# Kernel optimization log

Hardware: AMD Instinct MI355X
Metric: run time of the kernel (lower is better)

Reference implementation:

```python
import jax, jax.numpy as jnp
from jax import lax
import numpy as np

FEAT_STRIDE = 16
PRE_NMS_TOP_N = 2000
POST_NMS_TOP_N = 300
NMS_THRESH = 0.7


def _whctrs(a):
    w = a[2] - a[0] + 1.0
    h = a[3] - a[1] + 1.0
    return w, h, a[0] + 0.5 * (w - 1.0), a[1] + 0.5 * (h - 1.0)


def _mkanchors(ws, hs, x_ctr, y_ctr):
    ws = np.asarray(ws, dtype=np.float64)
    hs = np.asarray(hs, dtype=np.float64)
    return np.stack([x_ctr - 0.5 * (ws - 1.0), y_ctr - 0.5 * (hs - 1.0),
                     x_ctr + 0.5 * (ws - 1.0), y_ctr + 0.5 * (hs - 1.0)], axis=1)


def generate_anchors(base_size=16, ratios=np.array([0.5, 1.0, 2.0]), scales=np.array([8.0, 16.0, 32.0])):
    base = np.array([1.0, 1.0, float(base_size), float(base_size)]) - 1.0
    w, h, xc, yc = _whctrs(base)
    size = w * h
    ws = np.round(np.sqrt(size / ratios))
    hs = np.round(ws * ratios)
    ratio_anchors = _mkanchors(ws, hs, xc, yc)
    out = []
    for i in range(ratio_anchors.shape[0]):
        w_i, h_i, xc_i, yc_i = _whctrs(ratio_anchors[i])
        out.append(_mkanchors(w_i * scales, h_i * scales, xc_i, yc_i))
    return np.vstack(out).astype(np.float32)


ANCHORS = generate_anchors()  # [A=9, 4]
NUM_ANCHORS = ANCHORS.shape[0]


def _nms_keep(boxes, thresh):
    # boxes [N,4], already sorted by descending score; torchvision IoU convention.
    x1, y1, x2, y2 = boxes[:, 0], boxes[:, 1], boxes[:, 2], boxes[:, 3]
    areas = (x2 - x1) * (y2 - y1)
    xx1 = jnp.maximum(x1[:, None], x1[None, :])
    yy1 = jnp.maximum(y1[:, None], y1[None, :])
    xx2 = jnp.minimum(x2[:, None], x2[None, :])
    yy2 = jnp.minimum(y2[:, None], y2[None, :])
    inter = jnp.clip(xx2 - xx1, 0.0) * jnp.clip(yy2 - yy1, 0.0)
    iou = inter / (areas[:, None] + areas[None, :] - inter + 1e-9)
    n = boxes.shape[0]
    # sup[i, j] True => box i (higher score) suppresses later box j
    sup = (iou > thresh) & jnp.triu(jnp.ones((n, n), bool), 1)

    def body(i, keep):
        return keep & ~(keep[i] & sup[i])

    return lax.fori_loop(0, n, body, jnp.ones((n,), bool))


def setup_inputs() -> dict:
    key = jax.random.key(0)
    k1, k2 = jax.random.split(key)
    B, A, H, W = 8, NUM_ANCHORS, 128, 128
    scores = jax.random.normal(k1, (B, 2 * A, H, W), jnp.float32)
    bbox_deltas = jax.random.normal(k2, (B, 4 * A, H, W), jnp.float32) * 0.2
    im_h = float(H * FEAT_STRIDE)
    im_w = float(W * FEAT_STRIDE)
    im_info = jnp.tile(jnp.array([[im_h, im_w, 1.0]], jnp.float32), (B, 1))
    return {"scores": scores, "bbox_deltas": bbox_deltas, "im_info": im_info}


def reference(scores, bbox_deltas, im_info):
    B, _, H, W = scores.shape
    A = NUM_ANCHORS
    # --- anchor generation over the feature grid ---
    sx = jnp.arange(W, dtype=jnp.float32) * FEAT_STRIDE
    sy = jnp.arange(H, dtype=jnp.float32) * FEAT_STRIDE
    gx, gy = jnp.meshgrid(sx, sy)  # 'xy' indexing matches np.meshgrid default
    shifts = jnp.stack([gx.ravel(), gy.ravel(), gx.ravel(), gy.ravel()], axis=1)  # [K,4]
    anchors = (jnp.asarray(ANCHORS)[None, :, :] + shifts[:, None, :]).reshape(-1, 4)  # [K*A,4]

    obj_scores = scores[:, A:].transpose(0, 2, 3, 1).reshape(B, -1)   # [B, K*A]
    deltas = bbox_deltas.transpose(0, 2, 3, 1).reshape(B, -1, 4)      # [B, K*A, 4]

    # --- bbox_transform_inv ---
    widths = anchors[:, 2] - anchors[:, 0] + 1.0
    heights = anchors[:, 3] - anchors[:, 1] + 1.0
    ctr_x = anchors[:, 0] + 0.5 * widths
    ctr_y = anchors[:, 1] + 0.5 * heights
    dx, dy, dw, dh = deltas[..., 0], deltas[..., 1], deltas[..., 2], deltas[..., 3]
    pred_ctr_x = dx * widths + ctr_x
    pred_ctr_y = dy * heights + ctr_y
    pred_w = jnp.exp(dw) * widths
    pred_h = jnp.exp(dh) * heights
    proposals = jnp.stack([pred_ctr_x - 0.5 * pred_w, pred_ctr_y - 0.5 * pred_h,
                           pred_ctr_x + 0.5 * pred_w, pred_ctr_y + 0.5 * pred_h], axis=-1)

    # --- clip_boxes: im_info[b] = (h, w, scale) ---
    max_x = (im_info[:, 1] - 1.0)[:, None]
    max_y = (im_info[:, 0] - 1.0)[:, None]
    proposals = jnp.stack([
        jnp.clip(proposals[..., 0], 0.0, max_x),
        jnp.clip(proposals[..., 1], 0.0, max_y),
        jnp.clip(proposals[..., 2], 0.0, max_x),
        jnp.clip(proposals[..., 3], 0.0, max_y)], axis=-1)

    # --- pre-NMS top-k by score ---
    _, order = lax.top_k(obj_scores, PRE_NMS_TOP_N)                  # [B, pre]
    top_props = jnp.take_along_axis(proposals, order[..., None], axis=1)  # [B, pre, 4]

    # --- per-image greedy NMS (fixed-size, jit-compatible) ---
    keep = jax.vmap(lambda b: _nms_keep(b, NMS_THRESH))(top_props)   # [B, pre] bool
    sel = jnp.argsort(jnp.where(keep, 0, 1), axis=1, stable=True)[:, :POST_NMS_TOP_N]
    valid = jnp.take_along_axis(keep, sel, axis=1)                   # [B, post]
    out_boxes = jnp.take_along_axis(top_props, sel[..., None], axis=1) * valid[..., None].astype(top_props.dtype)

    batch_idx = jnp.broadcast_to(
        jnp.arange(B, dtype=out_boxes.dtype)[:, None, None], (B, POST_NMS_TOP_N, 1))
    return jnp.concatenate([batch_idx, out_boxes], axis=-1)  # [B, post_nms_topN, 5]
```

## Files before the change

### kernel.cpp

```cpp
#include <hip/hip_runtime.h>

#define NB 8
#define NA 9
#define HH 128
#define WW 128
#define NCELL (HH * WW)
#define NTOT (NCELL * NA)
#define PRE_K 2000
#define POST_K 300
#define CAP 4096
#define HBLK 9
#define NMS_TH 0.7f

__constant__ float c_aw[NA] = {184.f, 368.f, 736.f, 128.f, 256.f, 512.f, 88.f, 176.f, 352.f};
__constant__ float c_ah[NA] = {96.f, 192.f, 384.f, 128.f, 256.f, 512.f, 176.f, 352.f, 704.f};

__device__ __forceinline__ unsigned int sortable(float s) {
    unsigned int u = __float_as_uint(s);
    return (u & 0x80000000u) ? ~u : (u | 0x80000000u);
}

__device__ __forceinline__ unsigned long long shflx64(unsigned long long v, int m) {
    return __shfl_xor(v, m, 64);
}

__global__ __launch_bounds__(1024) void hist0_kernel(const float* __restrict__ scores,
                                                     unsigned int* __restrict__ h0out) {
    __shared__ unsigned int h[2048];
    int b = blockIdx.y, tid = threadIdx.x;
    h[tid] = 0; h[tid + 1024] = 0;
    __syncthreads();
    const float4* sp4 = (const float4*)(scores + (size_t)b * 18 * NCELL + (size_t)NA * NCELL);
    int base4 = blockIdx.x * 4096;
#pragma unroll
    for (int e = 0; e < 4; ++e) {
        float4 v = sp4[base4 + e * 1024 + tid];
        atomicAdd(&h[sortable(v.x) >> 21], 1u);
        atomicAdd(&h[sortable(v.y) >> 21], 1u);
        atomicAdd(&h[sortable(v.z) >> 21], 1u);
        atomicAdd(&h[sortable(v.w) >> 21], 1u);
    }
    __syncthreads();
    unsigned int* o = h0out + ((size_t)(b * HBLK + blockIdx.x)) * 2048;
    o[tid] = h[tid];
    o[tid + 1024] = h[tid + 1024];
}

__global__ __launch_bounds__(1024) void select0_kernel(const unsigned int* __restrict__ h0out,
                                                       uint2* __restrict__ state0,
                                                       unsigned int* __restrict__ gh1,
                                                       int* __restrict__ cnt) {
    __shared__ unsigned int thr[1024];
    int b = blockIdx.x, tid = threadIdx.x;
    if (tid < 128) gh1[b * 128 + tid] = 0;
    if (tid == 0) cnt[b] = 0;
    unsigned int c0 = 0, c1 = 0;
    for (int p = 0; p < HBLK; ++p) {
        const unsigned int* hp = h0out + ((size_t)(b * HBLK + p)) * 2048;
        uint2 v = *(const uint2*)&hp[2 * tid];
        c0 += v.x; c1 += v.y;
    }
    thr[tid] = c0 + c1;
    __syncthreads();
    for (int off = 1; off < 1024; off <<= 1) {
        unsigned int v = (tid + off < 1024) ? thr[tid + off] : 0u;
        __syncthreads();
        thr[tid] += v;
        __syncthreads();
    }
    unsigned int above = (tid < 1023) ? thr[tid + 1] : 0u;
    if (thr[tid] >= (unsigned)PRE_K && above < (unsigned)PRE_K) {
        if (above + c1 >= (unsigned)PRE_K)
            state0[b] = make_uint2((unsigned)(2 * tid + 1), (unsigned)(PRE_K)-above);
        else
            state0[b] = make_uint2((unsigned)(2 * tid), (unsigned)(PRE_K)-above - c1);
    }
}

__global__ __launch_bounds__(1024) void hist1_kernel(const float* __restrict__ scores,
                                                     const uint2* __restrict__ state0,
                                                     unsigned int* __restrict__ gh1) {
    __shared__ unsigned int h[128];
    int b = blockIdx.y, tid = threadIdx.x;
    if (tid < 128) h[tid] = 0;
    __syncthreads();
    unsigned int piv = state0[b].x;
    const float4* sp4 = (const float4*)(scores + (size_t)b * 18 * NCELL + (size_t)NA * NCELL);
    int base4 = blockIdx.x * 4096;
#pragma unroll
    for (int e = 0; e < 4; ++e) {
        float4 v = sp4[base4 + e * 1024 + tid];
        unsigned int u;
        u = sortable(v.x); if ((u >> 21) == piv) atomicAdd(&h[(u >> 14) & 127u], 1u);
        u = sortable(v.y); if ((u >> 21) == piv) atomicAdd(&h[(u >> 14) & 127u], 1u);
        u = sortable(v.z); if ((u >> 21) == piv) atomicAdd(&h[(u >> 14) & 127u], 1u);
        u = sortable(v.w); if ((u >> 21) == piv) atomicAdd(&h[(u >> 14) & 127u], 1u);
    }
    __syncthreads();
    if (tid < 128 && h[tid]) atomicAdd(&gh1[b * 128 + tid], h[tid]);
}

__global__ void select1_kernel(const unsigned int* __restrict__ gh1,
                               const uint2* __restrict__ state0,
                               unsigned int* __restrict__ state1) {
    int b = blockIdx.x, lane = threadIdx.x;
    unsigned int c0 = 0, c1 = 0;
    if (lane < 64) {
        c0 = gh1[b * 128 + 2 * lane];
        c1 = gh1[b * 128 + 2 * lane + 1];
    }
    unsigned int sum = c0 + c1;
#pragma unroll
    for (int off = 1; off < 64; off <<= 1) {
        unsigned int v = __shfl_down(sum, off, 64);
        if (lane + off < 64) sum += v;
    }
    unsigned int above = __shfl_down(sum, 1, 64);
    if (lane == 63) above = 0;
    unsigned int need0 = state0[b].y;
    if (sum >= need0 && above < need0) {
        unsigned int d = (above + c1 >= need0) ? (unsigned)(2 * lane + 1) : (unsigned)(2 * lane);
        unsigned int prefix = (state0[b].x << 7) | d;
        state1[b] = prefix << 14;
    }
}

__global__ void gather_kernel(const float* __restrict__ scores,
                              const unsigned int* __restrict__ state1,
                              int* __restrict__ cnt,
                              unsigned long long* __restrict__ buf) {
    __shared__ unsigned long long lbuf[2048];
    __shared__ int lcnt;
    __shared__ int gbase;
    int b = blockIdx.y;
    int tid = threadIdx.x;
    if (tid == 0) lcnt = 0;
    __syncthreads();
    unsigned int P = state1[b];
    const float4* sp4 = (const float4*)(scores + (size_t)b * 18 * NCELL + (size_t)NA * NCELL);
    int base4 = blockIdx.x * 512;
#pragma unroll
    for (int e = 0; e < 2; ++e) {
        int t4 = base4 + e * 256 + tid;
        float4 v = sp4[t4];
        float el[4] = {v.x, v.y, v.z, v.w};
#pragma unroll
        for (int j = 0; j < 4; ++j) {
            unsigned int u = sortable(el[j]);
            if (u >= P) {
                int idx4 = t4 * 4 + j;
                int a = idx4 >> 14;
                int cell = idx4 & 16383;
                unsigned int i = (unsigned int)cell * 9u + (unsigned int)a;
                int pos = atomicAdd(&lcnt, 1);
                lbuf[pos] = ((unsigned long long)u << 32) |
                            (unsigned long long)(0xFFFFFFFFu - i);
            }
        }
    }
    __syncthreads();
    if (tid == 0) gbase = atomicAdd(&cnt[b], lcnt);
    __syncthreads();
    int m = lcnt, gb = gbase;
    for (int t = tid; t < m; t += 256) {
        int g = gb + t;
        if (g < CAP) buf[(size_t)b * CAP + g] = lbuf[t];
    }
}

#define SHFL_STEP(J)                                                          \
    {                                                                         \
        int d_ = (J) >> 1;                                                    \
        bool keepMax = (((tid & d_) == 0) == (((2u * (unsigned)tid) & k) == 0)); \
        unsigned long long pa = shflx64(va, d_);                              \
        unsigned long long pb = shflx64(vb, d_);                              \
        va = keepMax ? (va > pa ? va : pa) : (va < pa ? va : pa);             \
        vb = keepMax ? (vb > pb ? vb : pb) : (vb < pb ? vb : pb);             \
    }
#define LOCAL_STEP()                                                          \
    {                                                                         \
        bool desc = (((2u * (unsigned)tid) & k) == 0);                        \
        unsigned long long lo = va < vb ? va : vb;                            \
        unsigned long long hi = va < vb ? vb : va;                            \
        va = desc ? hi : lo; vb = desc ? lo : hi;                             \
    }

__global__ __launch_bounds__(1024) void sort_kernel(const unsigned long long* __restrict__ buf,
                                                    const int* __restrict__ cnt,
                                                    unsigned int* __restrict__ topidx) {
    __shared__ unsigned long long s[CAP];
    int b = blockIdx.x;
    int tid = threadIdx.x;
    int n = min(cnt[b], CAP);
    const unsigned long long* src = buf + (size_t)b * CAP;
    if (n <= 2048) {
        unsigned long long va = (2 * tid < n) ? src[2 * tid] : 0ULL;
        unsigned long long vb = (2 * tid + 1 < n) ? src[2 * tid + 1] : 0ULL;
#pragma unroll
        for (unsigned k = 2; k <= 128; k <<= 1) {
#pragma unroll
            for (unsigned j = k >> 1; j >= 2; j >>= 1) SHFL_STEP(j)
            LOCAL_STEP()
        }
        for (unsigned k = 256; k <= 2048; k <<= 1) {
            s[2 * tid] = va; s[2 * tid + 1] = vb;
            __syncthreads();
            for (unsigned j = k >> 1; j >= 128; j >>= 1) {
                for (int t = tid; t < 2048; t += 1024) {
                    int ixj = t ^ (int)j;
                    if (ixj > t) {
                        unsigned long long x = s[t], y = s[ixj];
                        if ((((unsigned)t & k) == 0) ? (x < y) : (x > y)) { s[t] = y; s[ixj] = x; }
                    }
                }
                __syncthreads();
            }
            va = s[2 * tid]; vb = s[2 * tid + 1];
#pragma unroll
            for (unsigned j = 64; j >= 2; j >>= 1) SHFL_STEP(j)
            LOCAL_STEP()
        }
        s[2 * tid] = va; s[2 * tid + 1] = vb;
        __syncthreads();
    } else {
        for (int t = tid; t < CAP; t += 1024)
            s[t] = (t < n) ? src[t] : 0ULL;
        __syncthreads();
        for (int k = 2; k <= CAP; k <<= 1) {
            for (int j = k >> 1; j > 0; j >>= 1) {
                for (int t = tid; t < CAP; t += 1024) {
                    int ixj = t ^ j;
                    if (ixj > t) {
                        unsigned long long x = s[t], y = s[ixj];
                        if (((t & k) == 0) ? (x < y) : (x > y)) { s[t] = y; s[ixj] = x; }
                    }
                }
                __syncthreads();
            }
        }
    }
    for (int r = tid; r < PRE_K; r += 1024)
        topidx[(size_t)b * PRE_K + r] = 0xFFFFFFFFu - (unsigned int)(s[r] & 0xFFFFFFFFu);
}

__global__ void decode_kernel(const unsigned int* __restrict__ topidx,
                              const float* __restrict__ deltas,
                              const float* __restrict__ im_info,
                              float4* __restrict__ props) {
    int gid = blockIdx.x * 256 + threadIdx.x;
    if (gid >= NB * PRE_K) return;
    int b = gid / PRE_K;
    unsigned int i = topidx[gid];
    unsigned int cell = i / 9u;
    unsigned int a = i - cell * 9u;
    int wx = (int)(cell & 127u), hy = (int)(cell >> 7);
    const float* dp = deltas + (size_t)b * 36 * NCELL + (size_t)(4u * a) * NCELL +
                      (size_t)hy * WW + wx;
    float dx = dp[0];
    float dy = dp[NCELL];
    float dw = dp[2 * NCELL];
    float dh = dp[3 * NCELL];
    float W_ = c_aw[a], H_ = c_ah[a];
    float cx = (float)(16 * wx + 8), cy = (float)(16 * hy + 8);
    float px = __fadd_rn(__fmul_rn(dx, W_), cx);
    float py = __fadd_rn(__fmul_rn(dy, H_), cy);
    float pw = __fmul_rn((float)exp((double)dw), W_);
    float ph = __fmul_rn((float)exp((double)dh), H_);
    float hw = __fmul_rn(0.5f, pw), hh = __fmul_rn(0.5f, ph);
    float x1 = __fsub_rn(px, hw), y1 = __fsub_rn(py, hh);
    float x2 = __fadd_rn(px, hw), y2 = __fadd_rn(py, hh);
    float maxx = __fsub_rn(im_info[b * 3 + 1], 1.0f);
    float maxy = __fsub_rn(im_info[b * 3 + 0], 1.0f);
    x1 = fminf(fmaxf(x1, 0.0f), maxx);
    y1 = fminf(fmaxf(y1, 0.0f), maxy);
    x2 = fminf(fmaxf(x2, 0.0f), maxx);
    y2 = fminf(fmaxf(y2, 0.0f), maxy);
    props[gid] = make_float4(x1, y1, x2, y2);
}

__global__ void mask_kernel(const float4* __restrict__ boxes,
                            unsigned long long* __restrict__ colm) {
    int iT = blockIdx.x, jT = blockIdx.y, b = blockIdx.z;
    if (iT > jT) return;
    __shared__ float4 ib[64];
    int t = threadIdx.x;
    int i0 = iT * 64;
    ib[t] = (i0 + t < PRE_K) ? boxes[(size_t)b * PRE_K + i0 + t] : make_float4(0.f, 0.f, -1.f, -1.f);
    __syncthreads();
    int j = jT * 64 + t;
    if (j >= PRE_K) return;
    float4 jb = boxes[(size_t)b * PRE_K + j];
    float barea = __fmul_rn(__fsub_rn(jb.z, jb.x), __fsub_rn(jb.w, jb.y));
    unsigned long long m = 0ULL;
    for (int ii = 0; ii < 64; ++ii) {
        int i = i0 + ii;
        if (i < j) {
            float4 c = ib[ii];
            float aarea = __fmul_rn(__fsub_rn(c.z, c.x), __fsub_rn(c.w, c.y));
            float xx1 = fmaxf(c.x, jb.x), yy1 = fmaxf(c.y, jb.y);
            float xx2 = fminf(c.z, jb.z), yy2 = fminf(c.w, jb.w);
            float iw = fmaxf(__fsub_rn(xx2, xx1), 0.0f);
            float ih = fmaxf(__fsub_rn(yy2, yy1), 0.0f);
            float inter = __fmul_rn(iw, ih);
            float denom = __fadd_rn(__fsub_rn(__fadd_rn(aarea, barea), inter), 1e-9f);
            float iou = __fdiv_rn(inter, denom);
            if (iou > NMS_TH) m |= (1ULL << ii);
        }
    }
    colm[((size_t)b * 32 + iT) * 2048 + j] = m;
}

__global__ void scan_kernel(const unsigned long long* __restrict__ colm,
                            const float4* __restrict__ boxes,
                            float* __restrict__ out) {
    int b = blockIdx.x;
    int lane = threadIdx.x;
    __shared__ unsigned long long kw[32];
    __shared__ int keeplist[POST_K];
    const unsigned long long* cb = colm + (size_t)b * 32 * 2048;
    int total = 0;
    bool done = false;
    for (int k = 0; k < 32 && !done; ++k) {
        int j = k * 64 + lane;
        unsigned long long d = 0;
        int w = 0;
        for (; w + 4 <= k; w += 4) {
            unsigned long long a0 = cb[(size_t)(w + 0) * 2048 + j] & kw[w + 0];
            unsigned long long a1 = cb[(size_t)(w + 1) * 2048 + j] & kw[w + 1];
            unsigned long long a2 = cb[(size_t)(w + 2) * 2048 + j] & kw[w + 2];
            unsigned long long a3 = cb[(size_t)(w + 3) * 2048 + j] & kw[w + 3];
            d |= (a0 | a1) | (a2 | a3);
        }
        for (; w < k; ++w) d |= cb[(size_t)w * 2048 + j] & kw[w];
        unsigned long long diag = cb[(size_t)k * 2048 + j];
        bool alive_me = (d == 0ULL) && (j < PRE_K);
        unsigned long long alive = __ballot(alive_me);
        unsigned long long keptw = 0ULL;
        while (alive) {
            int i = __builtin_ctzll(alive);
            keptw |= (1ULL << i);
            if (lane == 0) keeplist[total] = k * 64 + i;
            total++;
            if (total >= POST_K) { done = true; break; }
            unsigned long long sup = __ballot(((diag >> i) & 1ULL) != 0ULL);
            alive &= ~sup;
            alive &= ~keptw;
        }
        if (lane == 0) kw[k] = keptw;
        __syncthreads();
    }
    __syncthreads();
    int K = min(total, POST_K);
    const float4* bb = boxes + (size_t)b * PRE_K;
    for (int r = lane; r < POST_K; r += 64) {
        float4 v = make_float4(0.f, 0.f, 0.f, 0.f);
        if (r < K) v = bb[keeplist[r]];
        float* o = out + ((size_t)b * POST_K + r) * 5;
        o[0] = (float)b;
        o[1] = v.x;
        o[2] = v.y;
        o[3] = v.z;
        o[4] = v.w;
    }
}

extern "C" void kernel_launch(void* const* d_in, const int* in_sizes, int n_in,
                              void* d_out, int out_size, void* d_ws, size_t ws_size,
                              hipStream_t stream) {
    const float* scores = (const float*)d_in[0];
    const float* deltas = (const float*)d_in[1];
    const float* im_info = (const float*)d_in[2];
    float* out = (float*)d_out;
    char* ws = (char*)d_ws;

    unsigned int* h0out = (unsigned int*)(ws + 0);
    unsigned int* gh1 = (unsigned int*)(ws + 589824);
    uint2* state0 = (uint2*)(ws + 593920);
    unsigned int* state1 = (unsigned int*)(ws + 593984);
    int* cnt = (int*)(ws + 594048);
    unsigned long long* buf = (unsigned long long*)(ws + 594112);
    unsigned int* topidx = (unsigned int*)(ws + 856256);
    float4* props = (float4*)(ws + 920256);
    unsigned long long* colm = (unsigned long long*)(ws + 1176320);

    hipLaunchKernelGGL(hist0_kernel, dim3(HBLK, NB), dim3(1024), 0, stream, scores, h0out);
    hipLaunchKernelGGL(select0_kernel, dim3(NB), dim3(1024), 0, stream, h0out, state0, gh1, cnt);
    hipLaunchKernelGGL(hist1_kernel, dim3(HBLK, NB), dim3(1024), 0, stream, scores, state0, gh1);
    hipLaunchKernelGGL(select1_kernel, dim3(NB), dim3(64), 0, stream, gh1, state0, state1);
    hipLaunchKernelGGL(gather_kernel, dim3(72, NB), dim3(256), 0, stream, scores, state1, cnt, buf);
    hipLaunchKernelGGL(sort_kernel, dim3(NB), dim3(1024), 0, stream, buf, cnt, topidx);
    hipLaunchKernelGGL(decode_kernel, dim3((NB * PRE_K + 255) / 256), dim3(256), 0, stream,
                       topidx, deltas, im_info, props);
    hipLaunchKernelGGL(mask_kernel, dim3(32, 32, NB), dim3(64), 0, stream, props, colm);
    hipLaunchKernelGGL(scan_kernel, dim3(NB), dim3(64), 0, stream, colm, props, out);
}
```

Measured before the change: 106.1 us.

## Fuse radix-select passes and replace mask+scan NMS with single-block lazy NMS

Merges the second histogram pass into the gather: it collects every candidate in the coarse pivot bucket and builds the fine histogram in the same read of the scores. The fine pivot selection, filtering, bitonic sort and box decode move into one kernel. The all-pairs IoU mask and scan kernels are replaced by one block per image that tests each 64-box tile only against already-kept boxes, plus the in-tile diagonal. The 1024-wide shared-memory scan in select0 becomes a wave-shuffle scan, and the histogram grid is doubled. This cuts launches, one full score read and the quadratic mask work, but it serialises NMS into 8 blocks and needs a larger candidate buffer that can overflow its caps.

```diff
diff --git a/kernel.cpp b/kernel.cpp
--- a/kernel.cpp
+++ b/kernel.cpp
@@ -2,14 +2,12 @@
 
 #define NB 8
 #define NA 9
-#define HH 128
-#define WW 128
-#define NCELL (HH * WW)
+#define NCELL (128 * 128)
 #define NTOT (NCELL * NA)
 #define PRE_K 2000
 #define POST_K 300
-#define CAP 4096
-#define HBLK 9
+#define CAP2 8192
+#define PARTS 18
 #define NMS_TH 0.7f
 
 __constant__ float c_aw[NA] = {184.f, 368.f, 736.f, 128.f, 256.f, 512.f, 88.f, 176.f, 352.f};
@@ -22,6 +20,17 @@
 
 __device__ __forceinline__ unsigned long long shflx64(unsigned long long v, int m) {
     return __shfl_xor(v, m, 64);
+}
+
+__device__ __forceinline__ bool iou_gt(float4 c, float4 jb, float barea) {
+    float aarea = __fmul_rn(__fsub_rn(c.z, c.x), __fsub_rn(c.w, c.y));
+    float xx1 = fmaxf(c.x, jb.x), yy1 = fmaxf(c.y, jb.y);
+    float xx2 = fminf(c.z, jb.z), yy2 = fminf(c.w, jb.w);
+    float iw = fmaxf(__fsub_rn(xx2, xx1), 0.0f);
+    float ih = fmaxf(__fsub_rn(yy2, yy1), 0.0f);
+    float inter = __fmul_rn(iw, ih);
+    float denom = __fadd_rn(__fsub_rn(__fadd_rn(aarea, barea), inter), 1e-9f);
+    return __fdiv_rn(inter, denom) > NMS_TH;
 }
 
 __global__ __launch_bounds__(1024) void hist0_kernel(const float* __restrict__ scores,
@@ -31,9 +40,9 @@
     h[tid] = 0; h[tid + 1024] = 0;
     __syncthreads();
     const float4* sp4 = (const float4*)(scores + (size_t)b * 18 * NCELL + (size_t)NA * NCELL);
-    int base4 = blockIdx.x * 4096;
-#pragma unroll
-    for (int e = 0; e < 4; ++e) {
+    int base4 = blockIdx.x * 2048;
+#pragma unroll
+    for (int e = 0; e < 2; ++e) {
         float4 v = sp4[base4 + e * 1024 + tid];
         atomicAdd(&h[sortable(v.x) >> 21], 1u);
         atomicAdd(&h[sortable(v.y) >> 21], 1u);
@@ -41,7 +50,7 @@
         atomicAdd(&h[sortable(v.w) >> 21], 1u);
     }
     __syncthreads();
-    unsigned int* o = h0out + ((size_t)(b * HBLK + blockIdx.x)) * 2048;
+    unsigned int* o = h0out + ((size_t)(b * PARTS + blockIdx.x)) * 2048;
     o[tid] = h[tid];
     o[tid + 1024] = h[tid + 1024];
 }
@@ -50,26 +59,37 @@
                                                        uint2* __restrict__ state0,
                                                        unsigned int* __restrict__ gh1,
                                                        int* __restrict__ cnt) {
+    __shared__ unsigned int wpart[16], wexcl[16];
     __shared__ unsigned int thr[1024];
     int b = blockIdx.x, tid = threadIdx.x;
+    int lane = tid & 63, wid = tid >> 6;
     if (tid < 128) gh1[b * 128 + tid] = 0;
     if (tid == 0) cnt[b] = 0;
     unsigned int c0 = 0, c1 = 0;
-    for (int p = 0; p < HBLK; ++p) {
-        const unsigned int* hp = h0out + ((size_t)(b * HBLK + p)) * 2048;
+    for (int p = 0; p < PARTS; ++p) {
+        const unsigned int* hp = h0out + ((size_t)(b * PARTS + p)) * 2048;
         uint2 v = *(const uint2*)&hp[2 * tid];
         c0 += v.x; c1 += v.y;
     }
-    thr[tid] = c0 + c1;
-    __syncthreads();
-    for (int off = 1; off < 1024; off <<= 1) {
-        unsigned int v = (tid + off < 1024) ? thr[tid + off] : 0u;
-        __syncthreads();
-        thr[tid] += v;
-        __syncthreads();
-    }
+    unsigned int sum = c0 + c1;
+#pragma unroll
+    for (int off = 1; off < 64; off <<= 1) {
+        unsigned int v = __shfl_down(sum, off, 64);
+        if (lane + off < 64) sum += v;
+    }
+    if (lane == 0) wpart[wid] = sum;
+    __syncthreads();
+    if (tid < 16) {
+        unsigned int e = 0;
+        for (int w = tid + 1; w < 16; ++w) e += wpart[w];
+        wexcl[tid] = e;
+    }
+    __syncthreads();
+    unsigned int self = sum + wexcl[wid];
+    thr[tid] = self;
+    __syncthreads();
     unsigned int above = (tid < 1023) ? thr[tid + 1] : 0u;
-    if (thr[tid] >= (unsigned)PRE_K && above < (unsigned)PRE_K) {
+    if (self >= (unsigned)PRE_K && above < (unsigned)PRE_K) {
         if (above + c1 >= (unsigned)PRE_K)
             state0[b] = make_uint2((unsigned)(2 * tid + 1), (unsigned)(PRE_K)-above);
         else
@@ -77,94 +97,51 @@
     }
 }
 
-__global__ __launch_bounds__(1024) void hist1_kernel(const float* __restrict__ scores,
-                                                     const uint2* __restrict__ state0,
-                                                     unsigned int* __restrict__ gh1) {
-    __shared__ unsigned int h[128];
+__global__ __launch_bounds__(1024) void gatherc_kernel(const float* __restrict__ scores,
+                                                       const uint2* __restrict__ state0,
+                                                       unsigned int* __restrict__ gh1,
+                                                       int* __restrict__ cnt,
+                                                       unsigned long long* __restrict__ buf) {
+    __shared__ unsigned long long lbuf[2048];
+    __shared__ unsigned int h128[128];
+    __shared__ int lmisc[2];
     int b = blockIdx.y, tid = threadIdx.x;
-    if (tid < 128) h[tid] = 0;
+    if (tid < 128) h128[tid] = 0;
+    if (tid == 0) lmisc[0] = 0;
     __syncthreads();
     unsigned int piv = state0[b].x;
+    unsigned int P = piv << 21;
     const float4* sp4 = (const float4*)(scores + (size_t)b * 18 * NCELL + (size_t)NA * NCELL);
-    int base4 = blockIdx.x * 4096;
-#pragma unroll
-    for (int e = 0; e < 4; ++e) {
-        float4 v = sp4[base4 + e * 1024 + tid];
-        unsigned int u;
-        u = sortable(v.x); if ((u >> 21) == piv) atomicAdd(&h[(u >> 14) & 127u], 1u);
-        u = sortable(v.y); if ((u >> 21) == piv) atomicAdd(&h[(u >> 14) & 127u], 1u);
-        u = sortable(v.z); if ((u >> 21) == piv) atomicAdd(&h[(u >> 14) & 127u], 1u);
-        u = sortable(v.w); if ((u >> 21) == piv) atomicAdd(&h[(u >> 14) & 127u], 1u);
-    }
-    __syncthreads();
-    if (tid < 128 && h[tid]) atomicAdd(&gh1[b * 128 + tid], h[tid]);
-}
-
-__global__ void select1_kernel(const unsigned int* __restrict__ gh1,
-                               const uint2* __restrict__ state0,
-                               unsigned int* __restrict__ state1) {
-    int b = blockIdx.x, lane = threadIdx.x;
-    unsigned int c0 = 0, c1 = 0;
-    if (lane < 64) {
-        c0 = gh1[b * 128 + 2 * lane];
-        c1 = gh1[b * 128 + 2 * lane + 1];
-    }
-    unsigned int sum = c0 + c1;
-#pragma unroll
-    for (int off = 1; off < 64; off <<= 1) {
-        unsigned int v = __shfl_down(sum, off, 64);
-        if (lane + off < 64) sum += v;
-    }
-    unsigned int above = __shfl_down(sum, 1, 64);
-    if (lane == 63) above = 0;
-    unsigned int need0 = state0[b].y;
-    if (sum >= need0 && above < need0) {
-        unsigned int d = (above + c1 >= need0) ? (unsigned)(2 * lane + 1) : (unsigned)(2 * lane);
-        unsigned int prefix = (state0[b].x << 7) | d;
-        state1[b] = prefix << 14;
-    }
-}
-
-__global__ void gather_kernel(const float* __restrict__ scores,
-                              const unsigned int* __restrict__ state1,
-                              int* __restrict__ cnt,
-                              unsigned long long* __restrict__ buf) {
-    __shared__ unsigned long long lbuf[2048];
-    __shared__ int lcnt;
-    __shared__ int gbase;
-    int b = blockIdx.y;
-    int tid = threadIdx.x;
-    if (tid == 0) lcnt = 0;
-    __syncthreads();
-    unsigned int P = state1[b];
-    const float4* sp4 = (const float4*)(scores + (size_t)b * 18 * NCELL + (size_t)NA * NCELL);
-    int base4 = blockIdx.x * 512;
+    int base4 = blockIdx.x * 2048;
 #pragma unroll
     for (int e = 0; e < 2; ++e) {
-        int t4 = base4 + e * 256 + tid;
+        int t4 = base4 + e * 1024 + tid;
         float4 v = sp4[t4];
         float el[4] = {v.x, v.y, v.z, v.w};
 #pragma unroll
         for (int j = 0; j < 4; ++j) {
             unsigned int u = sortable(el[j]);
             if (u >= P) {
+                if ((u >> 21) == piv) atomicAdd(&h128[(u >> 14) & 127u], 1u);
                 int idx4 = t4 * 4 + j;
                 int a = idx4 >> 14;
                 int cell = idx4 & 16383;
                 unsigned int i = (unsigned int)cell * 9u + (unsigned int)a;
-                int pos = atomicAdd(&lcnt, 1);
-                lbuf[pos] = ((unsigned long long)u << 32) |
-                            (unsigned long long)(0xFFFFFFFFu - i);
-            }
-        }
-    }
-    __syncthreads();
-    if (tid == 0) gbase = atomicAdd(&cnt[b], lcnt);
-    __syncthreads();
-    int m = lcnt, gb = gbase;
-    for (int t = tid; t < m; t += 256) {
+                int pos = atomicAdd(&lmisc[0], 1);
+                if (pos < 2048)
+                    lbuf[pos] = ((unsigned long long)u << 32) |
+                                (unsigned long long)(0xFFFFFFFFu - i);
+            }
+        }
+    }
+    __syncthreads();
+    if (tid < 128 && h128[tid]) atomicAdd(&gh1[b * 128 + tid], h128[tid]);
+    if (tid == 0) lmisc[1] = atomicAdd(&cnt[b], min(lmisc[0], 2048));
+    __syncthreads();
+    int m = min(lmisc[0], 2048), gb = lmisc[1];
+    for (int t = tid; t < m; t += 1024) {
         int g = gb + t;
-        if (g < CAP) buf[(size_t)b * CAP + g] = lbuf[t];
+        if (g < CAP2) buf[(size_t)b * CAP2 + g] = lbuf[t];
     }
 }
 
@@ -185,17 +162,55 @@
         va = desc ? hi : lo; vb = desc ? lo : hi;                             \
     }
 
-__global__ __launch_bounds__(1024) void sort_kernel(const unsigned long long* __restrict__ buf,
-                                                    const int* __restrict__ cnt,
-                                                    unsigned int* __restrict__ topidx) {
-    __shared__ unsigned long long s[CAP];
-    int b = blockIdx.x;
-    int tid = threadIdx.x;
-    int n = min(cnt[b], CAP);
-    const unsigned long long* src = buf + (size_t)b * CAP;
-    if (n <= 2048) {
-        unsigned long long va = (2 * tid < n) ? src[2 * tid] : 0ULL;
-        unsigned long long vb = (2 * tid + 1 < n) ? src[2 * tid + 1] : 0ULL;
+__global__ __launch_bounds__(1024) void sortdec_kernel(const unsigned long long* __restrict__ buf,
+                                                       const int* __restrict__ cnt,
+                                                       const uint2* __restrict__ state0,
+                                                       const unsigned int* __restrict__ gh1,
+                                                       const float* __restrict__ deltas,
+                                                       const float* __restrict__ im_info,
+                                                       float4* __restrict__ props) {
+    __shared__ unsigned long long s[4096];
+    __shared__ unsigned int spiv;
+    __shared__ int fcnt;
+    int b = blockIdx.x, tid = threadIdx.x;
+    if (tid == 0) fcnt = 0;
+    if (tid < 64) {
+        int lane = tid;
+        unsigned int c0 = gh1[b * 128 + 2 * lane];
+        unsigned int c1 = gh1[b * 128 + 2 * lane + 1];
+        unsigned int sum = c0 + c1;
+#pragma unroll
+        for (int off = 1; off < 64; off <<= 1) {
+            unsigned int v = __shfl_down(sum, off, 64);
+            if (lane + off < 64) sum += v;
+        }
+        unsigned int above = __shfl_down(sum, 1, 64);
+        if (lane == 63) above = 0;
+        unsigned int need0 = state0[b].y;
+        if (sum >= need0 && above < need0) {
+            unsigned int d = (above + c1 >= need0) ? (unsigned)(2 * lane + 1) : (unsigned)(2 * lane);
+            spiv = ((state0[b].x << 7) | d) << 14;
+        }
+    }
+    __syncthreads();
+    unsigned int P = spiv;
+    int n = min(cnt[b], CAP2);
+    const unsigned long long* src = buf + (size_t)b * CAP2;
+    for (int t = tid; t < n; t += 1024) {
+        unsigned long long e = src[t];
+        if ((unsigned int)(e >> 32) >= P) {
+            int pos = atomicAdd(&fcnt, 1);
+            if (pos < 4096) s[pos] = e;
+        }
+    }
+    __syncthreads();
+    int n2 = min(fcnt, 4096);
+    int SZ = (n2 <= 2048) ? 2048 : 4096;
+    for (int t = tid; t < SZ; t += 1024)
+        if (t >= n2) s[t] = 0ULL;
+    __syncthreads();
+    if (SZ == 2048) {
+        unsigned long long va = s[2 * tid], vb = s[2 * tid + 1];
 #pragma unroll
         for (unsigned k = 2; k <= 128; k <<= 1) {
 #pragma unroll
@@ -223,12 +238,9 @@
         s[2 * tid] = va; s[2 * tid + 1] = vb;
         __syncthreads();
     } else {
-        for (int t = tid; t < CAP; t += 1024)
-            s[t] = (t < n) ? src[t] : 0ULL;
-        __syncthreads();
-        for (int k = 2; k <= CAP; k <<= 1) {
+        for (int k = 2; k <= 4096; k <<= 1) {
             for (int j = k >> 1; j > 0; j >>= 1) {
-                for (int t = tid; t < CAP; t += 1024) {
+                for (int t = tid; t < 4096; t += 1024) {
                     int ixj = t ^ j;
                     if (ixj > t) {
                         unsigned long long x = s[t], y = s[ixj];
@@ -239,122 +251,103 @@
             }
         }
     }
-    for (int r = tid; r < PRE_K; r += 1024)
-        topidx[(size_t)b * PRE_K + r] = 0xFFFFFFFFu - (unsigned int)(s[r] & 0xFFFFFFFFu);
-}
-
-__global__ void decode_kernel(const unsigned int* __restrict__ topidx,
-                              const float* __restrict__ deltas,
-                              const float* __restrict__ im_info,
-                              float4* __restrict__ props) {
-    int gid = blockIdx.x * 256 + threadIdx.x;
-    if (gid >= NB * PRE_K) return;
-    int b = gid / PRE_K;
-    unsigned int i = topidx[gid];
-    unsigned int cell = i / 9u;
-    unsigned int a = i - cell * 9u;
-    int wx = (int)(cell & 127u), hy = (int)(cell >> 7);
-    const float* dp = deltas + (size_t)b * 36 * NCELL + (size_t)(4u * a) * NCELL +
-                      (size_t)hy * WW + wx;
-    float dx = dp[0];
-    float dy = dp[NCELL];
-    float dw = dp[2 * NCELL];
-    float dh = dp[3 * NCELL];
-    float W_ = c_aw[a], H_ = c_ah[a];
-    float cx = (float)(16 * wx + 8), cy = (float)(16 * hy + 8);
-    float px = __fadd_rn(__fmul_rn(dx, W_), cx);
-    float py = __fadd_rn(__fmul_rn(dy, H_), cy);
-    float pw = __fmul_rn((float)exp((double)dw), W_);
-    float ph = __fmul_rn((float)exp((double)dh), H_);
-    float hw = __fmul_rn(0.5f, pw), hh = __fmul_rn(0.5f, ph);
-    float x1 = __fsub_rn(px, hw), y1 = __fsub_rn(py, hh);
-    float x2 = __fadd_rn(px, hw), y2 = __fadd_rn(py, hh);
     float maxx = __fsub_rn(im_info[b * 3 + 1], 1.0f);
     float maxy = __fsub_rn(im_info[b * 3 + 0], 1.0f);
-    x1 = fminf(fmaxf(x1, 0.0f), maxx);
-    y1 = fminf(fmaxf(y1, 0.0f), maxy);
-    x2 = fminf(fmaxf(x2, 0.0f), maxx);
-    y2 = fminf(fmaxf(y2, 0.0f), maxy);
-    props[gid] = make_float4(x1, y1, x2, y2);
-}
-
-__global__ void mask_kernel(const float4* __restrict__ boxes,
-                            unsigned long long* __restrict__ colm) {
-    int iT = blockIdx.x, jT = blockIdx.y, b = blockIdx.z;
-    if (iT > jT) return;
-    __shared__ float4 ib[64];
-    int t = threadIdx.x;
-    int i0 = iT * 64;
-    ib[t] = (i0 + t < PRE_K) ? boxes[(size_t)b * PRE_K + i0 + t] : make_float4(0.f, 0.f, -1.f, -1.f);
-    __syncthreads();
-    int j = jT * 64 + t;
-    if (j >= PRE_K) return;
-    float4 jb = boxes[(size_t)b * PRE_K + j];
-    float barea = __fmul_rn(__fsub_rn(jb.z, jb.x), __fsub_rn(jb.w, jb.y));
-    unsigned long long m = 0ULL;
-    for (int ii = 0; ii < 64; ++ii) {
-        int i = i0 + ii;
-        if (i < j) {
-            float4 c = ib[ii];
-            float aarea = __fmul_rn(__fsub_rn(c.z, c.x), __fsub_rn(c.w, c.y));
-            float xx1 = fmaxf(c.x, jb.x), yy1 = fmaxf(c.y, jb.y);
-            float xx2 = fminf(c.z, jb.z), yy2 = fminf(c.w, jb.w);
-            float iw = fmaxf(__fsub_rn(xx2, xx1), 0.0f);
-            float ih = fmaxf(__fsub_rn(yy2, yy1), 0.0f);
-            float inter = __fmul_rn(iw, ih);
-            float denom = __fadd_rn(__fsub_rn(__fadd_rn(aarea, barea), inter), 1e-9f);
-            float iou = __fdiv_rn(inter, denom);
-            if (iou > NMS_TH) m |= (1ULL << ii);
-        }
-    }
-    colm[((size_t)b * 32 + iT) * 2048 + j] = m;
-}
-
-__global__ void scan_kernel(const unsigned long long* __restrict__ colm,
-                            const float4* __restrict__ boxes,
-                            float* __restrict__ out) {
-    int b = blockIdx.x;
-    int lane = threadIdx.x;
-    __shared__ unsigned long long kw[32];
-    __shared__ int keeplist[POST_K];
-    const unsigned long long* cb = colm + (size_t)b * 32 * 2048;
-    int total = 0;
-    bool done = false;
-    for (int k = 0; k < 32 && !done; ++k) {
-        int j = k * 64 + lane;
-        unsigned long long d = 0;
-        int w = 0;
-        for (; w + 4 <= k; w += 4) {
-            unsigned long long a0 = cb[(size_t)(w + 0) * 2048 + j] & kw[w + 0];
-            unsigned long long a1 = cb[(size_t)(w + 1) * 2048 + j] & kw[w + 1];
-            unsigned long long a2 = cb[(size_t)(w + 2) * 2048 + j] & kw[w + 2];
-            unsigned long long a3 = cb[(size_t)(w + 3) * 2048 + j] & kw[w + 3];
-            d |= (a0 | a1) | (a2 | a3);
-        }
-        for (; w < k; ++w) d |= cb[(size_t)w * 2048 + j] & kw[w];
-        unsigned long long diag = cb[(size_t)k * 2048 + j];
-        bool alive_me = (d == 0ULL) && (j < PRE_K);
-        unsigned long long alive = __ballot(alive_me);
-        unsigned long long keptw = 0ULL;
-        while (alive) {
-            int i = __builtin_ctzll(alive);
-            keptw |= (1ULL << i);
-            if (lane == 0) keeplist[total] = k * 64 + i;
-            total++;
-            if (total >= POST_K) { done = true; break; }
-            unsigned long long sup = __ballot(((diag >> i) & 1ULL) != 0ULL);
-            alive &= ~sup;
-            alive &= ~keptw;
-        }
-        if (lane == 0) kw[k] = keptw;
+    const float* dbase = deltas + (size_t)b * 36 * NCELL;
+    for (int r = tid; r < PRE_K; r += 1024) {
+        unsigned int i = 0xFFFFFFFFu - (unsigned int)(s[r] & 0xFFFFFFFFu);
+        unsigned int cell = i / 9u;
+        unsigned int a = i - cell * 9u;
+        int wx = (int)(cell & 127u), hy = (int)(cell >> 7);
+        const float* dp = dbase + (size_t)(4u * a) * NCELL + (size_t)hy * 128 + wx;
+        float dx = dp[0];
+        float dy = dp[NCELL];
+        float dw = dp[2 * NCELL];
+        float dh = dp[3 * NCELL];
+        float W_ = c_aw[a], H_ = c_ah[a];
+        float cx = (float)(16 * wx + 8), cy = (float)(16 * hy + 8);
+        float px = __fadd_rn(__fmul_rn(dx, W_), cx);
+        float py = __fadd_rn(__fmul_rn(dy, H_), cy);
+        float pw = __fmul_rn((float)exp((double)dw), W_);
+        float ph = __fmul_rn((float)exp((double)dh), H_);
+        float hw = __fmul_rn(0.5f, pw), hh = __fmul_rn(0.5f, ph);
+        float x1 = __fsub_rn(px, hw), y1 = __fsub_rn(py, hh);
+        float x2 = __fadd_rn(px, hw), y2 = __fadd_rn(py, hh);
+        x1 = fminf(fmaxf(x1, 0.0f), maxx);
+        y1 = fminf(fmaxf(y1, 0.0f), maxy);
+        x2 = fminf(fmaxf(x2, 0.0f), maxx);
+        y2 = fminf(fmaxf(y2, 0.0f), maxy);
+        props[(size_t)b * PRE_K + r] = make_float4(x1, y1, x2, y2);
+    }
+}
+
+__global__ __launch_bounds__(1024) void nms_kernel(const float4* __restrict__ props,
+                                                   float* __restrict__ out) {
+    __shared__ float4 sbox[PRE_K];
+    __shared__ float4 kbox[POST_K];
+    __shared__ unsigned long long colpart[16][64];
+    __shared__ unsigned long long deadmask[16];
+    __shared__ int ctl[2];
+    int b = blockIdx.x, tid = threadIdx.x;
+    int jl = tid & 63, w = tid >> 6;
+    for (int t = tid; t < PRE_K; t += 1024) sbox[t] = props[(size_t)b * PRE_K + t];
+    if (tid == 0) { ctl[0] = 0; ctl[1] = 0; }
+    __syncthreads();
+    for (int k = 0; k < 32; ++k) {
+        int j = k * 64 + jl;
+        bool jvalid = j < PRE_K;
+        float4 jb = jvalid ? sbox[j] : make_float4(0.f, 0.f, -1.f, -1.f);
+        float barea = __fmul_rn(__fsub_rn(jb.z, jb.x), __fsub_rn(jb.w, jb.y));
+        int T = ctl[0];
+        bool dead = false;
+        if (jvalid) {
+            for (int i = w; i < T; i += 16) {
+                if (iou_gt(kbox[i], jb, barea)) { dead = true; break; }
+            }
+        }
+        deadmask[w] = __ballot(dead);
+        unsigned long long part = 0ULL;
+        if (jvalid) {
+#pragma unroll
+            for (int q = 0; q < 4; ++q) {
+                int ii = 4 * w + q;
+                if (ii < jl) {
+                    if (iou_gt(sbox[k * 64 + ii], jb, barea)) part |= (1ULL << ii);
+                }
+            }
+        }
+        colpart[w][jl] = part;
         __syncthreads();
-    }
-    __syncthreads();
-    int K = min(total, POST_K);
-    const float4* bb = boxes + (size_t)b * PRE_K;
-    for (int r = lane; r < POST_K; r += 64) {
+        if (w == 0) {
+            unsigned long long d = deadmask[0];
+            unsigned long long diag = colpart[0][jl];
+#pragma unroll
+            for (int x = 1; x < 16; ++x) { d |= deadmask[x]; diag |= colpart[x][jl]; }
+            bool mydead = ((d >> jl) & 1ULL) != 0ULL;
+            unsigned long long alive = __ballot(!mydead && jvalid);
+            unsigned long long keptw = 0ULL;
+            int total = ctl[0];
+            int done = 0;
+            while (alive) {
+                int i = __builtin_ctzll(alive);
+                keptw |= (1ULL << i);
+                if (jl == 0 && total < POST_K) kbox[total] = sbox[k * 64 + i];
+                total++;
+                if (total >= POST_K) { done = 1; break; }
+                unsigned long long sup = __ballot(((diag >> i) & 1ULL) != 0ULL);
+                alive &= ~sup;
+                alive &= ~keptw;
+            }
+            if (jl == 0) { ctl[0] = total; ctl[1] = done; }
+        }
+        __syncthreads();
+        if (ctl[1]) break;
+    }
+    __syncthreads();
+    int K = min(ctl[0], POST_K);
+    for (int r = tid; r < POST_K; r += 1024) {
         float4 v = make_float4(0.f, 0.f, 0.f, 0.f);
-        if (r < K) v = bb[keeplist[r]];
+        if (r < K) v = kbox[r];
         float* o = out + ((size_t)b * POST_K + r) * 5;
         o[0] = (float)b;
         o[1] = v.x;
@@ -374,23 +367,17 @@
     char* ws = (char*)d_ws;
 
     unsigned int* h0out = (unsigned int*)(ws + 0);
-    unsigned int* gh1 = (unsigned int*)(ws + 589824);
-    uint2* state0 = (uint2*)(ws + 593920);
-    unsigned int* state1 = (unsigned int*)(ws + 593984);
-    int* cnt = (int*)(ws + 594048);
-    unsigned long long* buf = (unsigned long long*)(ws + 594112);
-    unsigned int* topidx = (unsigned int*)(ws + 856256);
-    float4* props = (float4*)(ws + 920256);
-    unsigned long long* colm = (unsigned long long*)(ws + 1176320);
-
-    hipLaunchKernelGGL(hist0_kernel, dim3(HBLK, NB), dim3(1024), 0, stream, scores, h0out);
+    unsigned int* gh1 = (unsigned int*)(ws + 1179648);
+    uint2* state0 = (uint2*)(ws + 1183744);
+    int* cnt = (int*)(ws + 1183808);
+    unsigned long long* buf = (unsigned long long*)(ws + 1183872);
+    float4* props = (float4*)(ws + 1708160);
+
+    hipLaunchKernelGGL(hist0_kernel, dim3(PARTS, NB), dim3(1024), 0, stream, scores, h0out);
     hipLaunchKernelGGL(select0_kernel, dim3(NB), dim3(1024), 0, stream, h0out, state0, gh1, cnt);
-    hipLaunchKernelGGL(hist1_kernel, dim3(HBLK, NB), dim3(1024), 0, stream, scores, state0, gh1);
-    hipLaunchKernelGGL(select1_kernel, dim3(NB), dim3(64), 0, stream, gh1, state0, state1);
-    hipLaunchKernelGGL(gather_kernel, dim3(72, NB), dim3(256), 0, stream, scores, state1, cnt, buf);
-    hipLaunchKernelGGL(sort_kernel, dim3(NB), dim3(1024), 0, stream, buf, cnt, topidx);
-    hipLaunchKernelGGL(decode_kernel, dim3((NB * PRE_K + 255) / 256), dim3(256), 0, stream,
-                       topidx, deltas, im_info, props);
-    hipLaunchKernelGGL(mask_kernel, dim3(32, 32, NB), dim3(64), 0, stream, props, colm);
-    hipLaunchKernelGGL(scan_kernel, dim3(NB), dim3(64), 0, stream, colm, props, out);
-}
+    hipLaunchKernelGGL(gatherc_kernel, dim3(PARTS, NB), dim3(1024), 0, stream,
+                       scores, state0, gh1, cnt, buf);
+    hipLaunchKernelGGL(sortdec_kernel, dim3(NB), dim3(1024), 0, stream,
+                       buf, cnt, state0, gh1, deltas, im_info, props);
+    hipLaunchKernelGGL(nms_kernel, dim3(NB), dim3(1024), 0, stream, props, out);
+}
```

After: 100.7 us. 5.1% less time.
